# Performance work log

Hardware: AMD Instinct MI355X
Metric: run time of the kernel (lower is better)

Reference implementation:

```python
import jax, jax.numpy as jnp
import numpy as np

D = 1024
H = 16
DH = D // H
SCALE = 1.0 / float(np.sqrt(DH))
EPS = 1e-5


def layer_norm(x, g, b):
    mu = jnp.mean(x, axis=-1, keepdims=True)
    var = jnp.mean((x - mu) ** 2, axis=-1, keepdims=True)
    return (x - mu) * jax.lax.rsqrt(var + EPS) * g + b


def setup_inputs() -> dict:
    key = jax.random.key(0)
    ks = jax.random.split(key, 12)
    B, N = 2, 2048
    x = jax.random.normal(ks[0], (B, N, D), dtype=jnp.float32)
    # sparse 0/1 adjacency (tree-like density) plus self loops
    adj = (jax.random.uniform(ks[1], (B, N, N)) < 0.002).astype(jnp.float32)
    adj = jnp.maximum(adj, jnp.eye(N, dtype=jnp.float32)[None])
    attn_mask = jnp.zeros((B, N, N), dtype=jnp.float32)
    s = 0.02
    params = {
        "qkv_w": jax.random.normal(ks[2], (D, 3 * D)) * s,
        "qkv_b": jnp.zeros((3 * D,), jnp.float32),
        "out_w": jax.random.normal(ks[3], (D, D)) * s,
        "out_b": jnp.zeros((D,), jnp.float32),
        "ln1_g": jnp.ones((D,), jnp.float32),
        "ln1_b": jnp.zeros((D,), jnp.float32),
        "ln2_g": jnp.ones((D,), jnp.float32),
        "ln2_b": jnp.zeros((D,), jnp.float32),
        "ff1_w": jax.random.normal(ks[4], (D, 4 * D)) * s,
        "ff1_b": jnp.zeros((4 * D,), jnp.float32),
        "ff2_w": jax.random.normal(ks[5], (4 * D, D)) * s,
        "ff2_b": jnp.zeros((D,), jnp.float32),
        "struct_bias": jnp.zeros((1,), jnp.float32) + 0.1,
    }
    return {"x": x, "adjacency": adj, "attn_mask": attn_mask, **params}


def reference(x, adjacency, attn_mask, qkv_w, qkv_b, out_w, out_b,
              ln1_g, ln1_b, ln2_g, ln2_b, ff1_w, ff1_b, ff2_w, ff2_b,
              struct_bias):
    b, n, d = x.shape
    residual = x
    h = layer_norm(x, ln1_g, ln1_b)
    qkv = (h @ qkv_w + qkv_b).reshape(b, n, 3, H, DH)
    q = jnp.transpose(qkv[:, :, 0], (0, 2, 1, 3))  # [B,H,N,Dh]
    k = jnp.transpose(qkv[:, :, 1], (0, 2, 1, 3))
    v = jnp.transpose(qkv[:, :, 2], (0, 2, 1, 3))
    scores = jnp.einsum("bhqd,bhkd->bhqk", q, k) * SCALE
    scores = scores + struct_bias[0] * adjacency[:, None] + attn_mask[:, None]
    attn = jax.nn.softmax(scores, axis=-1)  # dropout is identity at eval
    out = jnp.einsum("bhqk,bhkd->bhqd", attn, v)
    out = jnp.transpose(out, (0, 2, 1, 3)).reshape(b, n, d)
    out = out @ out_w + out_b
    x1 = residual + out
    h2 = layer_norm(x1, ln2_g, ln2_b)
    ff = jax.nn.gelu(h2 @ ff1_w + ff1_b, approximate=False) @ ff2_w + ff2_b
    return x1 + ff
```

## Files before the change

kernel.cpp:

```cpp
#include <hip/hip_runtime.h>
#include <math.h>

#define Dm 1024
#define Hh 16
#define DHh 64
#define Bb 2
#define Nn 2048
#define Rr 4096
#define SCALE_ 0.125f
#define EPS_ 1e-5f
#define SMAX_ 4.0f
#define LOG2E_ 1.4426950408889634f

typedef unsigned short u16;
typedef __attribute__((ext_vector_type(8))) short short8;
typedef __attribute__((ext_vector_type(4))) float f32x4;

__device__ __forceinline__ u16 f2bf(float f) {
  union { float f; unsigned u; } v; v.f = f;
  unsigned r = v.u + 0x7fffu + ((v.u >> 16) & 1u);
  return (u16)(r >> 16);
}
__device__ __forceinline__ float bf2f(u16 h) {
  union { unsigned u; float f; } v; v.u = ((unsigned)h) << 16;
  return v.f;
}
__device__ __forceinline__ unsigned pk2(float a, float b) {
  union { float f; unsigned u; } x, y; x.f = a; y.f = b;
  return (x.u >> 16) | (y.u & 0xffff0000u);
}

__device__ __forceinline__ void g2l16(const u16* g, const u16* l) {
  __builtin_amdgcn_global_load_lds(
      (const __attribute__((address_space(1))) void*)g,
      (__attribute__((address_space(3))) void*)l, 16, 0, 0);
}

__global__ void transpose_all(const float* __restrict__ qkv_w, const float* __restrict__ out_w,
                              const float* __restrict__ ff1_w, const float* __restrict__ ff2_w,
                              u16* __restrict__ qkvT, u16* __restrict__ outT,
                              u16* __restrict__ ff1T, u16* __restrict__ ff2T) {
  __shared__ float tile[32][33];
  int flat = blockIdx.x;
  const float* W; u16* WT; int K, N, local;
  if (flat < 3072)        { W = qkv_w; WT = qkvT; K = 1024; N = 3072; local = flat; }
  else if (flat < 4096)   { W = out_w; WT = outT; K = 1024; N = 1024; local = flat - 3072; }
  else if (flat < 8192)   { W = ff1_w; WT = ff1T; K = 1024; N = 4096; local = flat - 4096; }
  else                    { W = ff2_w; WT = ff2T; K = 4096; N = 1024; local = flat - 8192; }
  int nx = N / 32;
  int n0 = (local % nx) * 32, k0 = (local / nx) * 32;
  int tx = threadIdx.x, ty = threadIdx.y;
#pragma unroll
  for (int i = 0; i < 4; i++)
    tile[ty + 8 * i][tx] = W[(size_t)(k0 + ty + 8 * i) * N + n0 + tx];
  __syncthreads();
#pragma unroll
  for (int i = 0; i < 4; i++)
    WT[(size_t)(n0 + ty + 8 * i) * K + k0 + tx] = f2bf(tile[tx][ty + 8 * i]);
}

__global__ void bias_precompute(const float* __restrict__ adj, const float* __restrict__ mask,
                                const float* __restrict__ sbp, u16* __restrict__ bias16) {
  const float sb = sbp[0];
  const float C3 = -SMAX_ * LOG2E_;
  size_t i = ((size_t)blockIdx.x * 256 + threadIdx.x) * 8;
  float4 a0 = *(const float4*)(adj + i);
  float4 a1 = *(const float4*)(adj + i + 4);
  float4 m0 = *(const float4*)(mask + i);
  float4 m1 = *(const float4*)(mask + i + 4);
  ushort4 o0, o1;
  o0.x = f2bf(fmaf(fmaf(sb, a0.x, m0.x), LOG2E_, C3));
  o0.y = f2bf(fmaf(fmaf(sb, a0.y, m0.y), LOG2E_, C3));
  o0.z = f2bf(fmaf(fmaf(sb, a0.z, m0.z), LOG2E_, C3));
  o0.w = f2bf(fmaf(fmaf(sb, a0.w, m0.w), LOG2E_, C3));
  o1.x = f2bf(fmaf(fmaf(sb, a1.x, m1.x), LOG2E_, C3));
  o1.y = f2bf(fmaf(fmaf(sb, a1.y, m1.y), LOG2E_, C3));
  o1.z = f2bf(fmaf(fmaf(sb, a1.z, m1.z), LOG2E_, C3));
  o1.w = f2bf(fmaf(fmaf(sb, a1.w, m1.w), LOG2E_, C3));
  *(ushort4*)(bias16 + i) = o0;
  *(ushort4*)(bias16 + i + 4) = o1;
}

template <int BI>
__global__ void ln_kernel(const void* __restrict__ xin, const float* __restrict__ g,
                          const float* __restrict__ be, u16* __restrict__ out) {
  int row = blockIdx.x;
  int t = threadIdx.x;
  float4 v;
  if (BI) {
    ushort4 uv = ((const ushort4*)((const u16*)xin + (size_t)row * Dm))[t];
    v.x = bf2f(uv.x); v.y = bf2f(uv.y); v.z = bf2f(uv.z); v.w = bf2f(uv.w);
  } else {
    v = ((const float4*)((const float*)xin + (size_t)row * Dm))[t];
  }
  float s = v.x + v.y + v.z + v.w;
  float s2 = v.x * v.x + v.y * v.y + v.z * v.z + v.w * v.w;
#pragma unroll
  for (int o = 32; o > 0; o >>= 1) { s += __shfl_down(s, o); s2 += __shfl_down(s2, o); }
  __shared__ float sm[8];
  int w = t >> 6;
  if ((t & 63) == 0) { sm[w] = s; sm[4 + w] = s2; }
  __syncthreads();
  if (t == 0) {
    float a = sm[0] + sm[1] + sm[2] + sm[3];
    float a2 = sm[4] + sm[5] + sm[6] + sm[7];
    float mu = a * (1.f / Dm);
    sm[0] = mu;
    sm[1] = rsqrtf(a2 * (1.f / Dm) - mu * mu + EPS_);
  }
  __syncthreads();
  float mu = sm[0], rstd = sm[1];
  float4 gv = ((const float4*)g)[t];
  float4 bv = ((const float4*)be)[t];
  ushort4 o4;
  o4.x = f2bf((v.x - mu) * rstd * gv.x + bv.x);
  o4.y = f2bf((v.y - mu) * rstd * gv.y + bv.y);
  o4.z = f2bf((v.z - mu) * rstd * gv.z + bv.z);
  o4.w = f2bf((v.w - mu) * rstd * gv.w + bv.w);
  ((ushort4*)(out + (size_t)row * Dm))[t] = o4;
}

template <int MODE, int MI, int NI>
__global__ __launch_bounds__(256) void gemm_bt(
    const u16* __restrict__ A, const u16* __restrict__ BT,
    const float* __restrict__ bias, const void* __restrict__ res,
    void* __restrict__ Cout, u16* __restrict__ qb,
    u16* __restrict__ kb, u16* __restrict__ vb, int Ndim, int Kdim) {
  constexpr int TM = MI * 32, TN = NI * 32;
  constexpr int NS = (TM + TN) / 16;
  __shared__ u16 As[2][TM * 32];
  __shared__ u16 Bs[2][TN * 32];
  const int t = threadIdx.x;
  const int wave = t >> 6, lane = t & 63;
  const int wm = wave >> 1, wn = wave & 1;
  const int lr = lane & 15, lq = lane >> 4;
  const int flat = blockIdx.x + gridDim.x * blockIdx.y;
  constexpr int nMb = 4096 / TM;
  constexpr int mpx = nMb / 8;
  const int xcd = flat & 7;
  const int p = flat >> 3;
  const int m0 = (xcd * mpx + (p % mpx)) * TM;
  const int n0 = (p / mpx) * TN;

  auto stage = [&](int kt, int bsel) {
#pragma unroll
    for (int s = wave; s < NS; s += 4) {
      if (s < TM / 16)
        g2l16(A + (size_t)(m0 + s * 16 + (lane >> 2)) * Kdim + kt + (lane & 3) * 8,
              &As[bsel][(s * 16) * 32]);
      else
        g2l16(BT + (size_t)(n0 + (s - TM / 16) * 16 + (lane >> 2)) * Kdim + kt + (lane & 3) * 8,
              &Bs[bsel][((s - TM / 16) * 16) * 32]);
    }
  };

  f32x4 acc[MI][NI];
#pragma unroll
  for (int i = 0; i < MI; i++)
#pragma unroll
    for (int j = 0; j < NI; j++) acc[i][j] = (f32x4){0.f, 0.f, 0.f, 0.f};

  stage(0, 0);
  int cur = 0;
  for (int kt = 0; kt < Kdim; kt += 32) {
    __syncthreads();
    if (kt + 32 < Kdim) stage(kt + 32, cur ^ 1);
    short8 af[MI], bf[NI];
#pragma unroll
    for (int i = 0; i < MI; i++)
      af[i] = *(const short8*)&As[cur][(wm * (MI * 16) + i * 16 + lr) * 32 + lq * 8];
#pragma unroll
    for (int j = 0; j < NI; j++)
      bf[j] = *(const short8*)&Bs[cur][(wn * (NI * 16) + j * 16 + lr) * 32 + lq * 8];
#pragma unroll
    for (int i = 0; i < MI; i++)
#pragma unroll
      for (int j = 0; j < NI; j++)
        acc[i][j] = __builtin_amdgcn_mfma_f32_16x16x32_bf16(af[i], bf[j], acc[i][j], 0, 0, 0);
    cur ^= 1;
  }

#pragma unroll
  for (int i = 0; i < MI; i++) {
#pragma unroll
    for (int j = 0; j < NI; j++) {
#pragma unroll
      for (int r = 0; r < 4; r++) {
        int row = m0 + wm * (MI * 16) + i * 16 + lq * 4 + r;
        int col = n0 + wn * (NI * 16) + j * 16 + lr;
        float val = acc[i][j][r] + bias[col];
        if (MODE == 0) {
          int s = col >> 10, rem = col & 1023;
          int hh = rem >> 6, dh = rem & 63;
          int bi = row >> 11, ni = row & 2047;
          if (s == 2) {
            vb[(((size_t)bi * Hh + hh) * DHh + dh) * Nn + ni] = f2bf(val);
          } else {
            u16* dst = (s == 0) ? qb : kb;
            dst[(((size_t)bi * Hh + hh) * Nn + ni) * DHh + dh] = f2bf(val);
          }
        } else if (MODE == 1) {
          size_t o = (size_t)row * Ndim + col;
          ((u16*)Cout)[o] = f2bf(val + ((const float*)res)[o]);
        } else if (MODE == 3) {
          size_t o = (size_t)row * Ndim + col;
          ((float*)Cout)[o] = val + bf2f(((const u16*)res)[o]);
        } else {
          float u = val;
          float y2 = 1.5957691216f * fmaf(0.044715f * u, u * u, u);
          float gv = u / (1.f + __expf(-y2));
          size_t o = (size_t)row * Ndim + col;
          ((u16*)Cout)[o] = f2bf(gv);
        }
      }
    }
  }
}

__global__ __launch_bounds__(256) void attn_kernel(
    const u16* __restrict__ q, const u16* __restrict__ k, const u16* __restrict__ vT,
    const u16* __restrict__ bias16, u16* __restrict__ pO0, u16* __restrict__ pO1,
    float* __restrict__ pl) {
  const int qt = blockIdx.x, hb = blockIdx.y, kp = blockIdx.z;
  const int hh = hb & 15, b = hb >> 4;
  const int t = threadIdx.x, wave = t >> 6, lane = t & 63;
  const int lr = lane & 15, lq = lane >> 4;
  const size_t head_off = (((size_t)b * Hh + hh) * Nn) * DHh;
  const u16* Q = q + head_off;
  const u16* K = k + head_off;
  const u16* Vt = vT + head_off;
  const int q0 = qt * 128;
  const int kbase = kp * (Nn / 2);
  u16* pO = kp ? pO1 : pO0;

  __shared__ u16 Ks[2][64 * 64];
  __shared__ u16 VsT[2][64 * 64];
  __shared__ u16 Ps[4][32 * 72];

  short8 qf[2][2];
#pragma unroll
  for (int qs = 0; qs < 2; qs++) {
    const u16* Qr = Q + (size_t)(q0 + wave * 32 + qs * 16 + lr) * DHh;
    qf[qs][0] = *(const short8*)(Qr + lq * 8);
    qf[qs][1] = *(const short8*)(Qr + 32 + lq * 8);
  }
  f32x4 o_acc[2][4];
  float l_acc[2];
#pragma unroll
  for (int qs = 0; qs < 2; qs++) {
#pragma unroll
    for (int j = 0; j < 4; j++) o_acc[qs][j] = (f32x4){0.f, 0.f, 0.f, 0.f};
    l_acc[qs] = 0.f;
  }

  const int lsub = lane >> 3;
  const int xch = ((lane & 7) ^ lsub) * 8;

  auto stage = [&](int kt, int bsel) {
#pragma unroll
    for (int i = 0; i < 4; i++) {
      const int s = wave + i * 4;
      if (s < 8)
        g2l16(K + (size_t)(kt + s * 8 + lsub) * DHh + xch, &Ks[bsel][s * 512]);
      else
        g2l16(Vt + (size_t)((s - 8) * 8 + lsub) * Nn + kt + xch,
              &VsT[bsel][(s - 8) * 512]);
    }
  };

  const int rsw = ((lr >> 2) & 3) << 4;
  const int kx = lr & 7;
  const u16* bp = bias16 + ((size_t)b * Nn + q0 + wave * 32 + lr) * Nn;
  const float C1 = SCALE_ * LOG2E_;
  const int kend = kbase + Nn / 2;

  ushort4 bw[2][4];
#pragma unroll
  for (int qs = 0; qs < 2; qs++)
#pragma unroll
    for (int ns = 0; ns < 4; ns++)
      bw[qs][ns] = *(const ushort4*)(bp + (size_t)qs * 16 * Nn + kbase + ns * 16 + lq * 4);

  stage(kbase, 0);
  int cur = 0;
  for (int kt = kbase; kt < kend; kt += 64) {
    __syncthreads();
    if (kt + 64 < kend) stage(kt + 64, cur ^ 1);
    const u16* Kc = Ks[cur];
    const u16* Vc = VsT[cur];

    short8 kf[4][2];
#pragma unroll
    for (int ns = 0; ns < 4; ns++) {
      int R = ns * 16 + lr;
      kf[ns][0] = *(const short8*)&Kc[R * 64 + ((lq ^ kx) * 8)];
      kf[ns][1] = *(const short8*)&Kc[R * 64 + (((4 + lq) ^ kx) * 8)];
    }
    f32x4 s0[4], s1[4];
    __builtin_amdgcn_s_setprio(1);
#pragma unroll
    for (int ns = 0; ns < 4; ns++) {
      f32x4 z = (f32x4){0.f, 0.f, 0.f, 0.f};
      s0[ns] = __builtin_amdgcn_mfma_f32_16x16x32_bf16(kf[ns][0], qf[0][0], z, 0, 0, 0);
      s0[ns] = __builtin_amdgcn_mfma_f32_16x16x32_bf16(kf[ns][1], qf[0][1], s0[ns], 0, 0, 0);
      s1[ns] = __builtin_amdgcn_mfma_f32_16x16x32_bf16(kf[ns][0], qf[1][0], z, 0, 0, 0);
      s1[ns] = __builtin_amdgcn_mfma_f32_16x16x32_bf16(kf[ns][1], qf[1][1], s1[ns], 0, 0, 0);
    }
    __builtin_amdgcn_s_setprio(0);

    float p0[4][4], p1[4][4];
#pragma unroll
    for (int ns = 0; ns < 4; ns++) {
      p0[ns][0] = exp2f(fmaf(s0[ns][0], C1, bf2f(bw[0][ns].x)));
      p0[ns][1] = exp2f(fmaf(s0[ns][1], C1, bf2f(bw[0][ns].y)));
      p0[ns][2] = exp2f(fmaf(s0[ns][2], C1, bf2f(bw[0][ns].z)));
      p0[ns][3] = exp2f(fmaf(s0[ns][3], C1, bf2f(bw[0][ns].w)));
      p1[ns][0] = exp2f(fmaf(s1[ns][0], C1, bf2f(bw[1][ns].x)));
      p1[ns][1] = exp2f(fmaf(s1[ns][1], C1, bf2f(bw[1][ns].y)));
      p1[ns][2] = exp2f(fmaf(s1[ns][2], C1, bf2f(bw[1][ns].z)));
      p1[ns][3] = exp2f(fmaf(s1[ns][3], C1, bf2f(bw[1][ns].w)));
      l_acc[0] += (p0[ns][0] + p0[ns][1]) + (p0[ns][2] + p0[ns][3]);
      l_acc[1] += (p1[ns][0] + p1[ns][1]) + (p1[ns][2] + p1[ns][3]);
    }
    if (kt + 64 < kend) {
#pragma unroll
      for (int qs = 0; qs < 2; qs++)
#pragma unroll
        for (int ns = 0; ns < 4; ns++)
          bw[qs][ns] = *(const ushort4*)(bp + (size_t)qs * 16 * Nn + kt + 64 + ns * 16 + lq * 4);
    }
#pragma unroll
    for (int ns = 0; ns < 4; ns++) {
      int sc = ((ns ^ ((lr >> 2) & 3)) << 4) + lq * 4;
      uint2 w0, w1;
      w0.x = pk2(p0[ns][0], p0[ns][1]); w0.y = pk2(p0[ns][2], p0[ns][3]);
      w1.x = pk2(p1[ns][0], p1[ns][1]); w1.y = pk2(p1[ns][2], p1[ns][3]);
      *(uint2*)&Ps[wave][lr * 72 + sc] = w0;
      *(uint2*)&Ps[wave][(16 + lr) * 72 + sc] = w1;
    }
    short8 pf[2][2];
#pragma unroll
    for (int qs = 0; qs < 2; qs++) {
      pf[qs][0] = *(const short8*)&Ps[wave][(qs * 16 + lr) * 72 + ((lq * 8) ^ rsw)];
      pf[qs][1] = *(const short8*)&Ps[wave][(qs * 16 + lr) * 72 + ((32 + lq * 8) ^ rsw)];
    }
#pragma unroll
    for (int j = 0; j < 4; j++) {
      int R = j * 16 + lr;
      short8 vf0 = *(const short8*)&Vc[R * 64 + ((lq ^ kx) * 8)];
      short8 vf1 = *(const short8*)&Vc[R * 64 + (((4 + lq) ^ kx) * 8)];
      __builtin_amdgcn_s_setprio(1);
      o_acc[0][j] = __builtin_amdgcn_mfma_f32_16x16x32_bf16(pf[0][0], vf0, o_acc[0][j], 0, 0, 0);
      o_acc[0][j] = __builtin_amdgcn_mfma_f32_16x16x32_bf16(pf[0][1], vf1, o_acc[0][j], 0, 0, 0);
      o_acc[1][j] = __builtin_amdgcn_mfma_f32_16x16x32_bf16(pf[1][0], vf0, o_acc[1][j], 0, 0, 0);
      o_acc[1][j] = __builtin_amdgcn_mfma_f32_16x16x32_bf16(pf[1][1], vf1, o_acc[1][j], 0, 0, 0);
      __builtin_amdgcn_s_setprio(0);
    }
    cur ^= 1;
  }
#pragma unroll
  for (int qs = 0; qs < 2; qs++) {
    float l = l_acc[qs];
    l += __shfl_xor(l, 16);
    l += __shfl_xor(l, 32);
    if (lane < 16)
      pl[((size_t)(kp * Bb + b) * Hh + hh) * Nn + q0 + wave * 32 + qs * 16 + lr] = l;
#pragma unroll
    for (int r = 0; r < 4; r++) {
      int qrow = q0 + wave * 32 + qs * 16 + lq * 4 + r;
#pragma unroll
      for (int j = 0; j < 4; j++) {
        pO[((size_t)(b * Nn + qrow)) * Dm + hh * DHh + j * 16 + lr] =
            f2bf(o_acc[qs][j][r]);
      }
    }
  }
}

__global__ void attn_combine(const u16* __restrict__ pO0, const u16* __restrict__ pO1,
                             const float* __restrict__ pl, u16* __restrict__ ao) {
  int row = blockIdx.x;
  int t = threadIdx.x;
  int col = t * 4;
  int b = row >> 11, n = row & 2047, hh = col >> 6;
  size_t li = ((size_t)b * Hh + hh) * Nn + n;
  float inv = 1.f / (pl[li] + pl[(size_t)Bb * Hh * Nn + li]);
  ushort4 a0 = *(const ushort4*)(pO0 + (size_t)row * Dm + col);
  ushort4 a1 = *(const ushort4*)(pO1 + (size_t)row * Dm + col);
  ushort4 o;
  o.x = f2bf((bf2f(a0.x) + bf2f(a1.x)) * inv);
  o.y = f2bf((bf2f(a0.y) + bf2f(a1.y)) * inv);
  o.z = f2bf((bf2f(a0.z) + bf2f(a1.z)) * inv);
  o.w = f2bf((bf2f(a0.w) + bf2f(a1.w)) * inv);
  *(ushort4*)(ao + (size_t)row * Dm + col) = o;
}

extern "C" void kernel_launch(void* const* d_in, const int* in_sizes, int n_in,
                              void* d_out, int out_size, void* d_ws, size_t ws_size,
                              hipStream_t stream) {
  const float* x     = (const float*)d_in[0];
  const float* adj   = (const float*)d_in[1];
  const float* amask = (const float*)d_in[2];
  const float* qkv_w = (const float*)d_in[3];
  const float* qkv_b = (const float*)d_in[4];
  const float* out_w = (const float*)d_in[5];
  const float* out_b = (const float*)d_in[6];
  const float* ln1_g = (const float*)d_in[7];
  const float* ln1_b = (const float*)d_in[8];
  const float* ln2_g = (const float*)d_in[9];
  const float* ln2_b = (const float*)d_in[10];
  const float* ff1_w = (const float*)d_in[11];
  const float* ff1_b = (const float*)d_in[12];
  const float* ff2_w = (const float*)d_in[13];
  const float* ff2_b = (const float*)d_in[14];
  const float* sbias = (const float*)d_in[15];

  char* w = (char*)d_ws;
  const size_t MB = 1024 * 1024;
  u16* h      = (u16*)(w);
  u16* qb     = (u16*)(w + 8 * MB);
  u16* kb     = (u16*)(w + 16 * MB);
  u16* vb     = (u16*)(w + 24 * MB);
  u16* ao     = (u16*)(w + 32 * MB);
  float* pl   = (float*)(w + 40 * MB);
  u16* x1     = (u16*)(w + 40 * MB);
  u16* pO0    = (u16*)(w + 48 * MB);
  u16* pO1    = h;
  u16* qkvT   = (u16*)(w + 56 * MB);
  u16* outT   = (u16*)(w + 62 * MB);
  u16* ff1T   = (u16*)(w + 64 * MB);
  u16* ff2T   = (u16*)(w + 72 * MB);
  u16* bias16 = (u16*)(w + 80 * MB);
  u16* ffo    = qb;

  transpose_all<<<dim3(12288), dim3(32, 8), 0, stream>>>(
      qkv_w, out_w, ff1_w, ff2_w, qkvT, outT, ff1T, ff2T);

  bias_precompute<<<dim3((Bb * Nn * Nn) / (8 * 256)), dim3(256), 0, stream>>>(adj, amask, sbias, bias16);

  ln_kernel<0><<<dim3(Rr), dim3(256), 0, stream>>>(x, ln1_g, ln1_b, h);

  gemm_bt<0, 4, 4><<<dim3(3072 / 128, 4096 / 128), dim3(256), 0, stream>>>(
      h, qkvT, qkv_b, nullptr, nullptr, qb, kb, vb, 3072, 1024);

  attn_kernel<<<dim3(16, 32, 2), dim3(256), 0, stream>>>(qb, kb, vb, bias16, pO0, pO1, pl);

  attn_combine<<<dim3(Rr), dim3(256), 0, stream>>>(pO0, pO1, pl, ao);

  gemm_bt<1, 4, 2><<<dim3(1024 / 64, 4096 / 128), dim3(256), 0, stream>>>(
      ao, outT, out_b, x, (void*)x1, nullptr, nullptr, nullptr, 1024, 1024);

  ln_kernel<1><<<dim3(Rr), dim3(256), 0, stream>>>(x1, ln2_g, ln2_b, h);

  gemm_bt<2, 4, 4><<<dim3(4096 / 128, 4096 / 128), dim3(256), 0, stream>>>(
      h, ff1T, ff1_b, nullptr, (void*)ffo, nullptr, nullptr, nullptr, 4096, 1024);

  gemm_bt<3, 4, 2><<<dim3(1024 / 64, 4096 / 128), dim3(256), 0, stream>>>(
      ffo, ff2T, ff2_b, x1, d_out, nullptr, nullptr, nullptr, 1024, 4096);
}
```

Before: 452.0 us.

## Split attention keys four ways and pass P fragments via lane shuffles

```diff
diff --git a/kernel.cpp b/kernel.cpp
--- a/kernel.cpp
+++ b/kernel.cpp
@@ -220,7 +220,7 @@
 __global__ __launch_bounds__(256) void attn_kernel(
     const u16* __restrict__ q, const u16* __restrict__ k, const u16* __restrict__ vT,
     const u16* __restrict__ bias16, u16* __restrict__ pO0, u16* __restrict__ pO1,
-    float* __restrict__ pl) {
+    u16* __restrict__ pO2, u16* __restrict__ pO3, float* __restrict__ pl) {
   const int qt = blockIdx.x, hb = blockIdx.y, kp = blockIdx.z;
   const int hh = hb & 15, b = hb >> 4;
   const int t = threadIdx.x, wave = t >> 6, lane = t & 63;
@@ -230,12 +230,11 @@
   const u16* K = k + head_off;
   const u16* Vt = vT + head_off;
   const int q0 = qt * 128;
-  const int kbase = kp * (Nn / 2);
-  u16* pO = kp ? pO1 : pO0;
+  const int kbase = kp * (Nn / 4);
+  u16* pO = (kp == 0) ? pO0 : (kp == 1) ? pO1 : (kp == 2) ? pO2 : pO3;
 
   __shared__ u16 Ks[2][64 * 64];
   __shared__ u16 VsT[2][64 * 64];
-  __shared__ u16 Ps[4][32 * 72];
 
   short8 qf[2][2];
 #pragma unroll
@@ -268,11 +267,10 @@
     }
   };
 
-  const int rsw = ((lr >> 2) & 3) << 4;
   const int kx = lr & 7;
   const u16* bp = bias16 + ((size_t)b * Nn + q0 + wave * 32 + lr) * Nn;
   const float C1 = SCALE_ * LOG2E_;
-  const int kend = kbase + Nn / 2;
+  const int kend = kbase + Nn / 4;
 
   ushort4 bw[2][4];
 #pragma unroll
@@ -308,19 +306,21 @@
     }
     __builtin_amdgcn_s_setprio(0);
 
-    float p0[4][4], p1[4][4];
+    uint2 w_[2][4];
 #pragma unroll
     for (int ns = 0; ns < 4; ns++) {
-      p0[ns][0] = exp2f(fmaf(s0[ns][0], C1, bf2f(bw[0][ns].x)));
-      p0[ns][1] = exp2f(fmaf(s0[ns][1], C1, bf2f(bw[0][ns].y)));
-      p0[ns][2] = exp2f(fmaf(s0[ns][2], C1, bf2f(bw[0][ns].z)));
-      p0[ns][3] = exp2f(fmaf(s0[ns][3], C1, bf2f(bw[0][ns].w)));
-      p1[ns][0] = exp2f(fmaf(s1[ns][0], C1, bf2f(bw[1][ns].x)));
-      p1[ns][1] = exp2f(fmaf(s1[ns][1], C1, bf2f(bw[1][ns].y)));
-      p1[ns][2] = exp2f(fmaf(s1[ns][2], C1, bf2f(bw[1][ns].z)));
-      p1[ns][3] = exp2f(fmaf(s1[ns][3], C1, bf2f(bw[1][ns].w)));
-      l_acc[0] += (p0[ns][0] + p0[ns][1]) + (p0[ns][2] + p0[ns][3]);
-      l_acc[1] += (p1[ns][0] + p1[ns][1]) + (p1[ns][2] + p1[ns][3]);
+      float p00 = exp2f(fmaf(s0[ns][0], C1, bf2f(bw[0][ns].x)));
+      float p01 = exp2f(fmaf(s0[ns][1], C1, bf2f(bw[0][ns].y)));
+      float p02 = exp2f(fmaf(s0[ns][2], C1, bf2f(bw[0][ns].z)));
+      float p03 = exp2f(fmaf(s0[ns][3], C1, bf2f(bw[0][ns].w)));
+      float p10 = exp2f(fmaf(s1[ns][0], C1, bf2f(bw[1][ns].x)));
+      float p11 = exp2f(fmaf(s1[ns][1], C1, bf2f(bw[1][ns].y)));
+      float p12 = exp2f(fmaf(s1[ns][2], C1, bf2f(bw[1][ns].z)));
+      float p13 = exp2f(fmaf(s1[ns][3], C1, bf2f(bw[1][ns].w)));
+      l_acc[0] += (p00 + p01) + (p02 + p03);
+      l_acc[1] += (p10 + p11) + (p12 + p13);
+      w_[0][ns].x = pk2(p00, p01); w_[0][ns].y = pk2(p02, p03);
+      w_[1][ns].x = pk2(p10, p11); w_[1][ns].y = pk2(p12, p13);
     }
     if (kt + 64 < kend) {
 #pragma unroll
@@ -329,20 +329,21 @@
         for (int ns = 0; ns < 4; ns++)
           bw[qs][ns] = *(const ushort4*)(bp + (size_t)qs * 16 * Nn + kt + 64 + ns * 16 + lq * 4);
     }
-#pragma unroll
-    for (int ns = 0; ns < 4; ns++) {
-      int sc = ((ns ^ ((lr >> 2) & 3)) << 4) + lq * 4;
-      uint2 w0, w1;
-      w0.x = pk2(p0[ns][0], p0[ns][1]); w0.y = pk2(p0[ns][2], p0[ns][3]);
-      w1.x = pk2(p1[ns][0], p1[ns][1]); w1.y = pk2(p1[ns][2], p1[ns][3]);
-      *(uint2*)&Ps[wave][lr * 72 + sc] = w0;
-      *(uint2*)&Ps[wave][(16 + lr) * 72 + sc] = w1;
-    }
+    const int sb = ((lane & 16) << 1) + lr;
     short8 pf[2][2];
 #pragma unroll
     for (int qs = 0; qs < 2; qs++) {
-      pf[qs][0] = *(const short8*)&Ps[wave][(qs * 16 + lr) * 72 + ((lq * 8) ^ rsw)];
-      pf[qs][1] = *(const short8*)&Ps[wave][(qs * 16 + lr) * 72 + ((32 + lq * 8) ^ rsw)];
+#pragma unroll
+      for (int half = 0; half < 2; half++) {
+        unsigned a0 = (lq < 2) ? w_[qs][half * 2].x : w_[qs][half * 2 + 1].x;
+        unsigned a1 = (lq < 2) ? w_[qs][half * 2].y : w_[qs][half * 2 + 1].y;
+        uint4 u;
+        u.x = __shfl(a0, sb);
+        u.y = __shfl(a1, sb);
+        u.z = __shfl(a0, sb + 16);
+        u.w = __shfl(a1, sb + 16);
+        pf[qs][half] = *(short8*)&u;
+      }
     }
 #pragma unroll
     for (int j = 0; j < 4; j++) {
@@ -378,21 +379,26 @@
 }
 
 __global__ void attn_combine(const u16* __restrict__ pO0, const u16* __restrict__ pO1,
+                             const u16* __restrict__ pO2, const u16* __restrict__ pO3,
                              const float* __restrict__ pl, u16* __restrict__ ao) {
   int row = blockIdx.x;
   int t = threadIdx.x;
   int col = t * 4;
   int b = row >> 11, n = row & 2047, hh = col >> 6;
   size_t li = ((size_t)b * Hh + hh) * Nn + n;
-  float inv = 1.f / (pl[li] + pl[(size_t)Bb * Hh * Nn + li]);
-  ushort4 a0 = *(const ushort4*)(pO0 + (size_t)row * Dm + col);
-  ushort4 a1 = *(const ushort4*)(pO1 + (size_t)row * Dm + col);
-  ushort4 o;
-  o.x = f2bf((bf2f(a0.x) + bf2f(a1.x)) * inv);
-  o.y = f2bf((bf2f(a0.y) + bf2f(a1.y)) * inv);
-  o.z = f2bf((bf2f(a0.z) + bf2f(a1.z)) * inv);
-  o.w = f2bf((bf2f(a0.w) + bf2f(a1.w)) * inv);
-  *(ushort4*)(ao + (size_t)row * Dm + col) = o;
+  const size_t S = (size_t)Bb * Hh * Nn;
+  float inv = 1.f / (pl[li] + pl[S + li] + pl[2 * S + li] + pl[3 * S + li]);
+  size_t o = (size_t)row * Dm + col;
+  ushort4 a0 = *(const ushort4*)(pO0 + o);
+  ushort4 a1 = *(const ushort4*)(pO1 + o);
+  ushort4 a2 = *(const ushort4*)(pO2 + o);
+  ushort4 a3 = *(const ushort4*)(pO3 + o);
+  ushort4 ov;
+  ov.x = f2bf((bf2f(a0.x) + bf2f(a1.x) + bf2f(a2.x) + bf2f(a3.x)) * inv);
+  ov.y = f2bf((bf2f(a0.y) + bf2f(a1.y) + bf2f(a2.y) + bf2f(a3.y)) * inv);
+  ov.z = f2bf((bf2f(a0.z) + bf2f(a1.z) + bf2f(a2.z) + bf2f(a3.z)) * inv);
+  ov.w = f2bf((bf2f(a0.w) + bf2f(a1.w) + bf2f(a2.w) + bf2f(a3.w)) * inv);
+  *(ushort4*)(ao + o) = ov;
 }
 
 extern "C" void kernel_launch(void* const* d_in, const int* in_sizes, int n_in,
@@ -422,11 +428,13 @@
   u16* kb     = (u16*)(w + 16 * MB);
   u16* vb     = (u16*)(w + 24 * MB);
   u16* ao     = (u16*)(w + 32 * MB);
-  float* pl   = (float*)(w + 40 * MB);
   u16* x1     = (u16*)(w + 40 * MB);
   u16* pO0    = (u16*)(w + 48 * MB);
   u16* pO1    = h;
+  u16* pO2    = ao;
+  u16* pO3    = (u16*)(w + 40 * MB);
   u16* qkvT   = (u16*)(w + 56 * MB);
+  float* pl   = (float*)(w + 56 * MB);
   u16* outT   = (u16*)(w + 62 * MB);
   u16* ff1T   = (u16*)(w + 64 * MB);
   u16* ff2T   = (u16*)(w + 72 * MB);
@@ -443,9 +451,10 @@
   gemm_bt<0, 4, 4><<<dim3(3072 / 128, 4096 / 128), dim3(256), 0, stream>>>(
       h, qkvT, qkv_b, nullptr, nullptr, qb, kb, vb, 3072, 1024);
 
-  attn_kernel<<<dim3(16, 32, 2), dim3(256), 0, stream>>>(qb, kb, vb, bias16, pO0, pO1, pl);
-
-  attn_combine<<<dim3(Rr), dim3(256), 0, stream>>>(pO0, pO1, pl, ao);
+  attn_kernel<<<dim3(16, 32, 4), dim3(256), 0, stream>>>(qb, kb, vb, bias16,
+                                                         pO0, pO1, pO2, pO3, pl);
+
+  attn_combine<<<dim3(Rr), dim3(256), 0, stream>>>(pO0, pO1, pO2, pO3, pl, ao);
 
   gemm_bt<1, 4, 2><<<dim3(1024 / 64, 4096 / 128), dim3(256), 0, stream>>>(
       ao, outT, out_b, x, (void*)x1, nullptr, nullptr, nullptr, 1024, 1024);
```

New measurement: 469.5 us. 3.9% more time.
